# Kernel optimization log

Measured on AMD Instinct MI355X. Metric: run time of the kernel, lower is better.

The kernel has to match this reference:

```python
import jax, jax.numpy as jnp
import numpy as np

N, H, D, HDIM, HID = 768, 4, 3, 64, 64


def setup_inputs() -> dict:
    key = jax.random.key(0)
    ks = jax.random.split(key, 12)

    def w(k, shape, scale=None):
        s = (1.0 / np.sqrt(shape[0])) if scale is None else scale
        return (jax.random.normal(k, shape, jnp.float32) * s).astype(jnp.float32)

    d_in_e = H + 2 * (HDIM + H * H)  # 4 + 2*(64+16) = 164
    return {
        "x": jax.random.normal(ks[0], (N, H, D), jnp.float32),
        "h": jax.random.normal(ks[1], (N, HDIM), jnp.float32),
        "phi_e_w0": w(ks[2], (d_in_e, HID)), "phi_e_b0": jnp.zeros((HID,), jnp.float32),
        "phi_e_w1": w(ks[3], (HID, HID)), "phi_e_b1": jnp.zeros((HID,), jnp.float32),
        "phi_inf_w": w(ks[4], (HID, 1)), "phi_inf_b": jnp.zeros((1,), jnp.float32),
        "phi_x_w0": w(ks[5], (HID, HID)), "phi_x_b0": jnp.zeros((HID,), jnp.float32),
        "phi_x_w1": w(ks[6], (HID, HID)), "phi_x_b1": jnp.zeros((HID,), jnp.float32),
        "phi_x_w2": w(ks[7], (HID, H), scale=0.001), "phi_x_b2": jnp.zeros((H,), jnp.float32),
        "phi_h_w0": w(ks[8], (HID + HDIM, HID)), "phi_h_b0": jnp.zeros((HID,), jnp.float32),
        "phi_h_w1": w(ks[9], (HID, HID)), "phi_h_b1": jnp.zeros((HID,), jnp.float32),
        "phi_h_w2": w(ks[10], (HID, HDIM)), "phi_h_b2": jnp.zeros((HDIM,), jnp.float32),
    }


def _mlp2(z, w0, b0, w1, b1):
    # hk.nets.MLP([HID, HID], activation=silu, activate_final=True)
    return jax.nn.silu(jax.nn.silu(z @ w0 + b0) @ w1 + b1)


def reference(x, h,
              phi_e_w0, phi_e_b0, phi_e_w1, phi_e_b1,
              phi_inf_w, phi_inf_b,
              phi_x_w0, phi_x_b0, phi_x_w1, phi_x_b1, phi_x_w2, phi_x_b2,
              phi_h_w0, phi_h_b0, phi_h_w1, phi_h_b1, phi_h_w2, phi_h_b2):
    n, n_heads = x.shape[0], x.shape[1]
    avg_num_neighbours = n - 1
    off_n = 1.0 - jnp.eye(n, dtype=x.dtype)          # zero node-diagonal mask

    # per-node head-pair differences: [n, H, H, 3], entry [m,i,j] = x[m,j]-x[m,i]
    diff_heads = x[:, None, :, :] - x[:, :, None, :]
    sq_norms_heads = jnp.sum(diff_heads ** 2, axis=-1)            # [n, H, H]
    h_concat = jnp.concatenate([h, sq_norms_heads.reshape(n, n_heads * n_heads)], axis=-1)

    # all-pairs node features: [n, n, 2*(HDIM+H^2)], entry [i,j] = [h_concat[j], h_concat[i]]
    hc_dim = h_concat.shape[-1]
    h_combos = jnp.concatenate([
        jnp.broadcast_to(h_concat[None, :, :], (n, n, hc_dim)),
        jnp.broadcast_to(h_concat[:, None, :], (n, n, hc_dim)),
    ], axis=-1)

    # all-pairs node differences per head: [n, n, H, 3], entry [i,j] = x[j]-x[i]
    diff_nodes = x[None, :, :, :] - x[:, None, :, :]
    sq_norms_nodes = jnp.sum(diff_nodes ** 2, axis=-1)            # [n, n, H]

    e_in = jnp.concatenate([sq_norms_nodes, h_combos], axis=-1)   # [n, n, 164]
    m_ij = _mlp2(e_in, phi_e_w0, phi_e_b0, phi_e_w1, phi_e_b1)    # [n, n, HID]
    m_ij = m_ij * off_n[:, :, None]

    e = jax.nn.sigmoid(m_ij @ phi_inf_w + phi_inf_b)[..., 0] * off_n  # [n, n]
    m_i = jnp.einsum('ijd,ij->id', m_ij, e) / jnp.sqrt(jnp.asarray(avg_num_neighbours, x.dtype))

    # phi_x: MLP(silu, activate_final) -> Linear(H) (tanh=False)
    phi_x_out = (_mlp2(m_ij, phi_x_w0, phi_x_b0, phi_x_w1, phi_x_b1) @ phi_x_w2 + phi_x_b2)
    phi_x_out = phi_x_out * off_n[:, :, None]                     # [n, n, H]

    # normalize_by_x_norm=True, normalization_constant=1.0
    norm = jnp.sqrt(jnp.where(sq_norms_nodes == 0.0, 1.0, sq_norms_nodes)) + 1.0
    norm_diff = (diff_nodes / norm[..., None]) * off_n[:, :, None, None]
    equivariant_shift = jnp.einsum('ijhd,ijh->ihd', norm_diff, phi_x_out)
    equivariant_shift = equivariant_shift / avg_num_neighbours    # agg='mean'

    x_new = x + equivariant_shift

    phi_h_in = jnp.concatenate([m_i, h], axis=-1)
    h_new = _mlp2(phi_h_in, phi_h_w0, phi_h_b0, phi_h_w1, phi_h_b1) @ phi_h_w2 + phi_h_b2
    h_new = h + h_new                                             # residual_h=True
    return (x_new, h_new)
```

## Files before the change

### kernel.cpp

```cpp
#include <hip/hip_runtime.h>
#include <hip/hip_bf16.h>
#include <math.h>

#define WS_BJ    0
#define WS_BI    49152
#define WS_W0AT  98304
#define WS_BIAS  98560
#define WS_INFW  98784
#define WS_WG    98848
#define WS_PM    106016
#define WS_PS    253472

typedef unsigned short ushort_t;
typedef __attribute__((ext_vector_type(8))) __bf16 bf16x8;
typedef __attribute__((ext_vector_type(4))) float f32x4;

__device__ __forceinline__ float silu_f(float v) {
    return v * __builtin_amdgcn_rcpf(1.0f + __expf(-v));
}
__device__ __forceinline__ float sigm_f(float v) {
    return __builtin_amdgcn_rcpf(1.0f + __expf(-v));
}

__device__ __forceinline__ ushort_t bf16r(float f) {
    unsigned u = __float_as_uint(f);
    u += 0x7FFFu + ((u >> 16) & 1u);
    return (ushort_t)(u >> 16);
}
__device__ __forceinline__ float bf2f(ushort_t s) { return __uint_as_float(((unsigned)s) << 16); }

__device__ __forceinline__ unsigned pk2(float a, float b) {
    __hip_bfloat162 t = __float22bfloat162_rn(make_float2(a, b));
    return *reinterpret_cast<unsigned*>(&t);
}

__global__ __launch_bounds__(256) void prep_kernel(
    const float* __restrict__ x, const float* __restrict__ h,
    const float* __restrict__ ew0, const float* __restrict__ eb0,
    const float* __restrict__ ew1, const float* __restrict__ eb1,
    const float* __restrict__ infw, const float* __restrict__ infb,
    const float* __restrict__ xw0, const float* __restrict__ xb0,
    const float* __restrict__ xw1, const float* __restrict__ xb1,
    const float* __restrict__ xw2, const float* __restrict__ xb2,
    float* __restrict__ ws)
{
    const int blk = blockIdx.x, tid = threadIdx.x;
    const int wv = tid >> 6, t = tid & 63;
    if (blk < 192) {
        __shared__ float hcs[4][80];
        const int m = blk * 4 + wv;
        hcs[wv][t] = h[m * 64 + t];
        if (t < 16) {
            int i2 = t >> 2, j2 = t & 3;
            float d0 = x[m*12 + j2*3 + 0] - x[m*12 + i2*3 + 0];
            float d1 = x[m*12 + j2*3 + 1] - x[m*12 + i2*3 + 1];
            float d2 = x[m*12 + j2*3 + 2] - x[m*12 + i2*3 + 2];
            hcs[wv][64 + t] = d0*d0 + d1*d1 + d2*d2;
        }
        float bj = 0.0f, bi = eb0[t];
        #pragma unroll 4
        for (int k = 0; k < 80; ++k) {
            float hv = hcs[wv][k];
            bj += hv * ew0[(4 + k) * 64 + t];
            bi += hv * ew0[(84 + k) * 64 + t];
        }
        ws[WS_BJ + m * 64 + t] = bj;
        ws[WS_BI + m * 64 + t] = bi;
    } else if (blk == 192) {
        if (wv == 0) {
            #pragma unroll
            for (int hh = 0; hh < 4; ++hh) ws[WS_W0AT + t * 4 + hh] = ew0[hh * 64 + t];
            ws[WS_INFW + t] = infw[t];
            #pragma unroll
            for (int u = 0; u < 4; ++u) {
                int idx = u * 64 + t;
                if (idx < 224) {
                    float v;
                    if (idx < 64)        v = eb1[idx];
                    else if (idx < 128)  v = xb0[idx - 64];
                    else if (idx == 128) v = infb[0];
                    else if (idx < 144)  v = 0.0f;
                    else if (idx < 208)  v = xb1[idx - 144];
                    else if (idx < 212)  v = xb2[idx - 208];
                    else                 v = 0.0f;
                    ws[WS_BIAS + idx] = v;
                }
            }
        }
    } else {
        ushort_t* wg = (ushort_t*)(ws + WS_WG);
        #pragma unroll 1
        for (int u = 0; u < 8; ++u) {
            int e = (blk - 193) * 2048 + tid * 8 + u;
            int r = e >> 6, k = e & 63;
            float v;
            if (r < 64)        v = ew1[k * 64 + r];
            else if (r < 128)  v = xw0[k * 64 + (r - 64)];
            else if (r == 128) v = infw[k];
            else if (r < 144)  v = 0.0f;
            else if (r < 208)  v = xw1[k * 64 + (r - 144)];
            else if (r < 212)  v = xw2[k * 4 + (r - 208)];
            else               v = 0.0f;
            wg[e] = bf16r(v);
        }
    }
}

__device__ __forceinline__ void load_bfrags(const ushort_t* yb, int ml, int q, bf16x8 B[4][2]) {
    #pragma unroll
    for (int pt = 0; pt < 4; ++pt)
        #pragma unroll
        for (int kt = 0; kt < 2; ++kt)
            B[pt][kt] = *(const bf16x8*)(yb + (pt*16 + ml) * 72 + kt*32 + q*8);
}

template<int NMT>
__device__ __forceinline__ void gemmG(const ushort_t* __restrict__ wg, int ml, int q,
                                      const bf16x8 B[4][2], f32x4* acc) {
    #pragma unroll
    for (int mt = 0; mt < NMT; ++mt) {
        #pragma unroll
        for (int kt = 0; kt < 2; ++kt) {
            bf16x8 af = *(const bf16x8*)(wg + (mt*16 + ml) * 64 + kt*32 + q*8);
            #pragma unroll
            for (int pt = 0; pt < 4; ++pt)
                acc[mt*4 + pt] = __builtin_amdgcn_mfma_f32_16x16x32_bf16(af, B[pt][kt], acc[mt*4 + pt], 0, 0, 0);
        }
    }
}

__device__ __forceinline__ void ep_silu2(ushort_t* yb, int ml, int q,
                                         const f32x4* acc, const float* __restrict__ bias,
                                         int coff) {
    #pragma unroll
    for (int mt = 0; mt < 2; ++mt) {
        float4 bv = *(const float4*)(bias + coff + mt*16 + q*4);
        #pragma unroll
        for (int pt = 0; pt < 4; ++pt) {
            f32x4 a = acc[mt*4 + pt];
            uint2 w = make_uint2(pk2(silu_f(a[0] + bv.x), silu_f(a[1] + bv.y)),
                                 pk2(silu_f(a[2] + bv.z), silu_f(a[3] + bv.w)));
            *(uint2*)(yb + (pt*16 + ml) * 72 + coff + mt*16 + q*4) = w;
        }
    }
}

__device__ __forceinline__ void layer64(ushort_t* yb, const ushort_t* __restrict__ wg,
                                        const float* __restrict__ bias, int ml, int q) {
    bf16x8 B[4][2];
    load_bfrags(yb, ml, q, B);
    f32x4 acc[8];
    #pragma unroll
    for (int t = 0; t < 8; ++t) acc[t] = f32x4{0.f, 0.f, 0.f, 0.f};
    gemmG<2>(wg, ml, q, B, acc);
    ep_silu2(yb, ml, q, acc, bias, 0);
    #pragma unroll
    for (int t = 0; t < 8; ++t) acc[t] = f32x4{0.f, 0.f, 0.f, 0.f};
    gemmG<2>(wg + 32*64, ml, q, B, acc);
    ep_silu2(yb, ml, q, acc, bias, 32);
}

__global__ __launch_bounds__(256, 2) void egcl_chunk(
    const float* __restrict__ x, float* __restrict__ ws)
{
    __shared__ ushort_t ybuf[4][4608];
    __shared__ float sbuf[4][64];
    __shared__ float redm[4][64];
    __shared__ float reds[4][12];

    const int it = blockIdx.x, i = blockIdx.y, tid = threadIdx.x;
    const int wv = tid >> 6, lane = tid & 63;
    const int ml = lane & 15, q = lane >> 4;
    const int jg = it * 256 + wv * 64 + lane;

    const ushort_t* wg = (const ushort_t*)(ws + WS_WG);
    const float* bias  = ws + WS_BIAS;
    const float* infwf = ws + WS_INFW;
    ushort_t* yb = ybuf[wv];

    float xi[12];
    #pragma unroll
    for (int t = 0; t < 12; ++t) xi[t] = x[i * 12 + t];

    float sqn[4];
    {
        const float4* xp = (const float4*)(x + jg * 12);
        float4 a = xp[0], b = xp[1], c = xp[2];
        float d0, d1, d2;
        d0=a.x-xi[0]; d1=a.y-xi[1]; d2=a.z-xi[2];   sqn[0]=d0*d0+d1*d1+d2*d2;
        d0=a.w-xi[3]; d1=b.x-xi[4]; d2=b.y-xi[5];   sqn[1]=d0*d0+d1*d1+d2*d2;
        d0=b.z-xi[6]; d1=b.w-xi[7]; d2=c.x-xi[8];   sqn[2]=d0*d0+d1*d1+d2*d2;
        d0=c.y-xi[9]; d1=c.z-xi[10];d2=c.w-xi[11];  sqn[3]=d0*d0+d1*d1+d2*d2;
    }

    {
        const float* Bi   = ws + WS_BI + i * 64;
        const float* w0at = ws + WS_W0AT;
        const float* Bj   = ws + WS_BJ + jg * 64;
        #pragma unroll
        for (int b = 0; b < 8; ++b) {
            float4 A = *(const float4*)(Bj + b*8);
            float4 Bv = *(const float4*)(Bj + b*8 + 4);
            float z[8] = {A.x, A.y, A.z, A.w, Bv.x, Bv.y, Bv.z, Bv.w};
            #pragma unroll
            for (int u = 0; u < 8; ++u) {
                int l = b*8 + u;
                float v = Bi[l] + z[u]
                        + sqn[0]*w0at[l*4+0] + sqn[1]*w0at[l*4+1]
                        + sqn[2]*w0at[l*4+2] + sqn[3]*w0at[l*4+3];
                z[u] = silu_f(v);
            }
            uint4 pkv = make_uint4(pk2(z[0],z[1]), pk2(z[2],z[3]),
                                   pk2(z[4],z[5]), pk2(z[6],z[7]));
            *(uint4*)(yb + lane * 72 + b*8) = pkv;
        }
    }

    layer64(yb, wg + 0, bias + 0, ml, q);

    {
        float sv = bias[128];
        #pragma unroll
        for (int c = 0; c < 8; ++c) {
            uint2 w0 = *(const uint2*)(yb + lane * 72 + c*8);
            uint2 w1 = *(const uint2*)(yb + lane * 72 + c*8 + 4);
            sv += __uint_as_float(w0.x << 16)          * infwf[c*8 + 0];
            sv += __uint_as_float(w0.x & 0xFFFF0000u)  * infwf[c*8 + 1];
            sv += __uint_as_float(w0.y << 16)          * infwf[c*8 + 2];
            sv += __uint_as_float(w0.y & 0xFFFF0000u)  * infwf[c*8 + 3];
            sv += __uint_as_float(w1.x << 16)          * infwf[c*8 + 4];
            sv += __uint_as_float(w1.x & 0xFFFF0000u)  * infwf[c*8 + 5];
            sv += __uint_as_float(w1.y << 16)          * infwf[c*8 + 6];
            sv += __uint_as_float(w1.y & 0xFFFF0000u)  * infwf[c*8 + 7];
        }
        sbuf[wv][lane] = (jg == i) ? 0.0f : sigm_f(sv);
    }

    float macc = 0.0f;
    #pragma unroll 8
    for (int j2 = 0; j2 < 64; ++j2) {
        float ev = sbuf[wv][j2];
        macc += ev * bf2f(yb[j2 * 72 + lane]);
    }

    layer64(yb, wg + 64*64, bias + 64, ml, q);
    layer64(yb, wg + 144*64, bias + 144, ml, q);

    float* yf = (float*)yb;
    {
        bf16x8 B[4][2];
        load_bfrags(yb, ml, q, B);
        f32x4 acc2[4];
        #pragma unroll
        for (int t = 0; t < 4; ++t) acc2[t] = f32x4{0.f, 0.f, 0.f, 0.f};
        gemmG<1>(wg + 208*64, ml, q, B, acc2);
        if (q == 0) {
            float4 bx2 = *(const float4*)(bias + 208);
            #pragma unroll
            for (int pt = 0; pt < 4; ++pt) {
                float4 pv = make_float4(acc2[pt][0] + bx2.x, acc2[pt][1] + bx2.y,
                                        acc2[pt][2] + bx2.z, acc2[pt][3] + bx2.w);
                *(float4*)(yf + (pt*16 + ml) * 4) = pv;
            }
        }
    }

    {
        float4 pv = *(const float4*)(yf + lane * 4);
        float pvh[4] = {pv.x, pv.y, pv.z, pv.w};
        float mask = (jg == i) ? 0.0f : 1.0f;
        const float4* xp = (const float4*)(x + jg * 12);
        float4 a = xp[0], b = xp[1], c = xp[2];
        float dxs[12];
        dxs[0]=a.x-xi[0]; dxs[1]=a.y-xi[1]; dxs[2]=a.z-xi[2];  dxs[3]=a.w-xi[3];
        dxs[4]=b.x-xi[4]; dxs[5]=b.y-xi[5]; dxs[6]=b.z-xi[6];  dxs[7]=b.w-xi[7];
        dxs[8]=c.x-xi[8]; dxs[9]=c.y-xi[9]; dxs[10]=c.z-xi[10];dxs[11]=c.w-xi[11];
        float s12[12];
        #pragma unroll
        for (int hh = 0; hh < 4; ++hh) {
            float nsq = (sqn[hh] == 0.0f) ? 1.0f : sqn[hh];
            float inv = mask * pvh[hh] * __builtin_amdgcn_rcpf(sqrtf(nsq) + 1.0f);
            #pragma unroll
            for (int d = 0; d < 3; ++d)
                s12[hh*3 + d] = dxs[hh*3 + d] * inv;
        }
        #pragma unroll
        for (int t = 0; t < 12; ++t) {
            float v = s12[t];
            v += __shfl_xor(v, 1, 64);
            v += __shfl_xor(v, 2, 64);
            v += __shfl_xor(v, 4, 64);
            v += __shfl_xor(v, 8, 64);
            v += __shfl_xor(v, 16, 64);
            v += __shfl_xor(v, 32, 64);
            if (lane == 0) reds[wv][t] = v;
        }
    }

    redm[wv][lane] = macc;
    __syncthreads();

    if (wv == 0) {
        ws[WS_PM + (i*3 + it)*64 + lane] =
            redm[0][lane] + redm[1][lane] + redm[2][lane] + redm[3][lane];
        if (lane < 12)
            ws[WS_PS + (i*3 + it)*12 + lane] =
                reds[0][lane] + reds[1][lane] + reds[2][lane] + reds[3][lane];
    }
}

__global__ __launch_bounds__(256) void finish_kernel(
    const float* __restrict__ x, const float* __restrict__ h,
    const float* __restrict__ hw0, const float* __restrict__ hb0,
    const float* __restrict__ hw1, const float* __restrict__ hb1,
    const float* __restrict__ hw2, const float* __restrict__ hb2,
    const float* __restrict__ ws, float* __restrict__ out)
{
    __shared__ float inbuf[4][128];
    __shared__ float zbuf[4][64];
    const int tid = threadIdx.x;
    const int wv = tid >> 6, lane = tid & 63;
    const int i = blockIdx.x * 4 + wv;

    const float* pm = ws + WS_PM + i*3*64;
    float mi = (pm[lane] + pm[64 + lane] + pm[128 + lane]) * (1.0f / sqrtf(767.0f));
    inbuf[wv][lane] = mi;
    inbuf[wv][64 + lane] = h[i*64 + lane];

    if (lane < 12) {
        const float* ps = ws + WS_PS + i*3*12;
        float sh = ps[lane] + ps[12 + lane] + ps[24 + lane];
        out[i*12 + lane] = x[i*12 + lane] + sh * (1.0f / 767.0f);
    }

    float a = hb0[lane];
    #pragma unroll 8
    for (int k = 0; k < 128; ++k) a += inbuf[wv][k] * hw0[k*64 + lane];
    zbuf[wv][lane] = silu_f(a);

    a = hb1[lane];
    #pragma unroll 8
    for (int k = 0; k < 64; ++k) a += zbuf[wv][k] * hw1[k*64 + lane];
    zbuf[wv][lane] = silu_f(a);

    a = hb2[lane];
    #pragma unroll 8
    for (int k = 0; k < 64; ++k) a += zbuf[wv][k] * hw2[k*64 + lane];
    out[9216 + i*64 + lane] = h[i*64 + lane] + a;
}

extern "C" void kernel_launch(void* const* d_in, const int* in_sizes, int n_in,
                              void* d_out, int out_size, void* d_ws, size_t ws_size,
                              hipStream_t stream) {
    const float* x    = (const float*)d_in[0];
    const float* h    = (const float*)d_in[1];
    const float* ew0  = (const float*)d_in[2];
    const float* eb0  = (const float*)d_in[3];
    const float* ew1  = (const float*)d_in[4];
    const float* eb1  = (const float*)d_in[5];
    const float* infw = (const float*)d_in[6];
    const float* infb = (const float*)d_in[7];
    const float* xw0  = (const float*)d_in[8];
    const float* xb0  = (const float*)d_in[9];
    const float* xw1  = (const float*)d_in[10];
    const float* xb1  = (const float*)d_in[11];
    const float* xw2  = (const float*)d_in[12];
    const float* xb2  = (const float*)d_in[13];
    const float* hw0  = (const float*)d_in[14];
    const float* hb0  = (const float*)d_in[15];
    const float* hw1  = (const float*)d_in[16];
    const float* hb1  = (const float*)d_in[17];
    const float* hw2  = (const float*)d_in[18];
    const float* hb2  = (const float*)d_in[19];

    float* ws  = (float*)d_ws;
    float* out = (float*)d_out;

    prep_kernel<<<200, 256, 0, stream>>>(x, h, ew0, eb0, ew1, eb1, infw, infb,
                                         xw0, xb0, xw1, xb1, xw2, xb2, ws);
    egcl_chunk<<<dim3(3, 768), 256, 0, stream>>>(x, ws);
    finish_kernel<<<192, 256, 0, stream>>>(x, h, hw0, hb0, hw1, hb1, hw2, hb2, ws, out);
}
```

Baseline: 171.8 us.

## Swizzle LDS activation tiles, fold bias into MFMA accumulators, use 192-thread blocks

```diff
diff --git a/kernel.cpp b/kernel.cpp
--- a/kernel.cpp
+++ b/kernel.cpp
@@ -9,7 +9,7 @@
 #define WS_INFW  98784
 #define WS_WG    98848
 #define WS_PM    106016
-#define WS_PS    253472
+#define WS_PS    302624
 
 typedef unsigned short ushort_t;
 typedef __attribute__((ext_vector_type(8))) __bf16 bf16x8;
@@ -32,6 +32,13 @@
 __device__ __forceinline__ unsigned pk2(float a, float b) {
     __hip_bfloat162 t = __float22bfloat162_rn(make_float2(a, b));
     return *reinterpret_cast<unsigned*>(&t);
+}
+
+__device__ __forceinline__ int ybo(int row, int slot) {
+    return row * 64 + (((slot) ^ (row & 7)) << 3);
+}
+__device__ __forceinline__ int yfo(int row) {
+    return row * 32 + ((row & 7) << 2);
 }
 
 __global__ __launch_bounds__(256) void prep_kernel(
@@ -111,7 +118,7 @@
     for (int pt = 0; pt < 4; ++pt)
         #pragma unroll
         for (int kt = 0; kt < 2; ++kt)
-            B[pt][kt] = *(const bf16x8*)(yb + (pt*16 + ml) * 72 + kt*32 + q*8);
+            B[pt][kt] = *(const bf16x8*)(yb + ybo(pt*16 + ml, kt*4 + q));
 }
 
 template<int NMT>
@@ -130,17 +137,17 @@
 }
 
 __device__ __forceinline__ void ep_silu2(ushort_t* yb, int ml, int q,
-                                         const f32x4* acc, const float* __restrict__ bias,
-                                         int coff) {
+                                         const f32x4* acc, int coff) {
     #pragma unroll
     for (int mt = 0; mt < 2; ++mt) {
-        float4 bv = *(const float4*)(bias + coff + mt*16 + q*4);
         #pragma unroll
         for (int pt = 0; pt < 4; ++pt) {
             f32x4 a = acc[mt*4 + pt];
-            uint2 w = make_uint2(pk2(silu_f(a[0] + bv.x), silu_f(a[1] + bv.y)),
-                                 pk2(silu_f(a[2] + bv.z), silu_f(a[3] + bv.w)));
-            *(uint2*)(yb + (pt*16 + ml) * 72 + coff + mt*16 + q*4) = w;
+            uint2 w = make_uint2(pk2(silu_f(a[0]), silu_f(a[1])),
+                                 pk2(silu_f(a[2]), silu_f(a[3])));
+            int row  = pt*16 + ml;
+            int slot = (coff >> 3) + mt*2 + (q >> 1);
+            *(uint2*)(yb + ybo(row, slot) + (q & 1) * 4) = w;
         }
     }
 }
@@ -151,27 +158,35 @@
     load_bfrags(yb, ml, q, B);
     f32x4 acc[8];
     #pragma unroll
-    for (int t = 0; t < 8; ++t) acc[t] = f32x4{0.f, 0.f, 0.f, 0.f};
+    for (int mt = 0; mt < 2; ++mt) {
+        float4 bv = *(const float4*)(bias + mt*16 + q*4);
+        #pragma unroll
+        for (int pt = 0; pt < 4; ++pt) acc[mt*4 + pt] = f32x4{bv.x, bv.y, bv.z, bv.w};
+    }
     gemmG<2>(wg, ml, q, B, acc);
-    ep_silu2(yb, ml, q, acc, bias, 0);
-    #pragma unroll
-    for (int t = 0; t < 8; ++t) acc[t] = f32x4{0.f, 0.f, 0.f, 0.f};
+    ep_silu2(yb, ml, q, acc, 0);
+    #pragma unroll
+    for (int mt = 0; mt < 2; ++mt) {
+        float4 bv = *(const float4*)(bias + 32 + mt*16 + q*4);
+        #pragma unroll
+        for (int pt = 0; pt < 4; ++pt) acc[mt*4 + pt] = f32x4{bv.x, bv.y, bv.z, bv.w};
+    }
     gemmG<2>(wg + 32*64, ml, q, B, acc);
-    ep_silu2(yb, ml, q, acc, bias, 32);
-}
-
-__global__ __launch_bounds__(256, 2) void egcl_chunk(
+    ep_silu2(yb, ml, q, acc, 32);
+}
+
+__global__ __launch_bounds__(192, 4) void egcl_chunk(
     const float* __restrict__ x, float* __restrict__ ws)
 {
-    __shared__ ushort_t ybuf[4][4608];
-    __shared__ float sbuf[4][64];
-    __shared__ float redm[4][64];
-    __shared__ float reds[4][12];
+    __shared__ __align__(16) ushort_t ybuf[3][4096];
+    __shared__ float sbuf[3][64];
+    __shared__ float redm[3][64];
+    __shared__ float reds[3][12];
 
     const int it = blockIdx.x, i = blockIdx.y, tid = threadIdx.x;
     const int wv = tid >> 6, lane = tid & 63;
     const int ml = lane & 15, q = lane >> 4;
-    const int jg = it * 256 + wv * 64 + lane;
+    const int jg = it * 192 + wv * 64 + lane;
 
     const ushort_t* wg = (const ushort_t*)(ws + WS_WG);
     const float* bias  = ws + WS_BIAS;
@@ -212,7 +227,7 @@
             }
             uint4 pkv = make_uint4(pk2(z[0],z[1]), pk2(z[2],z[3]),
                                    pk2(z[4],z[5]), pk2(z[6],z[7]));
-            *(uint4*)(yb + lane * 72 + b*8) = pkv;
+            *(uint4*)(yb + ybo(lane, b)) = pkv;
         }
     }
 
@@ -222,8 +237,9 @@
         float sv = bias[128];
         #pragma unroll
         for (int c = 0; c < 8; ++c) {
-            uint2 w0 = *(const uint2*)(yb + lane * 72 + c*8);
-            uint2 w1 = *(const uint2*)(yb + lane * 72 + c*8 + 4);
+            int base = ybo(lane, c);
+            uint2 w0 = *(const uint2*)(yb + base);
+            uint2 w1 = *(const uint2*)(yb + base + 4);
             sv += __uint_as_float(w0.x << 16)          * infwf[c*8 + 0];
             sv += __uint_as_float(w0.x & 0xFFFF0000u)  * infwf[c*8 + 1];
             sv += __uint_as_float(w0.y << 16)          * infwf[c*8 + 2];
@@ -237,10 +253,13 @@
     }
 
     float macc = 0.0f;
-    #pragma unroll 8
-    for (int j2 = 0; j2 < 64; ++j2) {
-        float ev = sbuf[wv][j2];
-        macc += ev * bf2f(yb[j2 * 72 + lane]);
+    {
+        const int g = lane >> 3, l7 = lane & 7;
+        #pragma unroll 8
+        for (int j2 = 0; j2 < 64; ++j2) {
+            float ev = sbuf[wv][j2];
+            macc += ev * bf2f(yb[j2*64 + (((g ^ (j2 & 7)) << 3) + l7)]);
+        }
     }
 
     layer64(yb, wg + 64*64, bias + 64, ml, q);
@@ -251,22 +270,22 @@
         bf16x8 B[4][2];
         load_bfrags(yb, ml, q, B);
         f32x4 acc2[4];
-        #pragma unroll
-        for (int t = 0; t < 4; ++t) acc2[t] = f32x4{0.f, 0.f, 0.f, 0.f};
+        float4 bx2 = *(const float4*)(bias + 208);
+        #pragma unroll
+        for (int t = 0; t < 4; ++t) acc2[t] = f32x4{bx2.x, bx2.y, bx2.z, bx2.w};
         gemmG<1>(wg + 208*64, ml, q, B, acc2);
         if (q == 0) {
-            float4 bx2 = *(const float4*)(bias + 208);
             #pragma unroll
             for (int pt = 0; pt < 4; ++pt) {
-                float4 pv = make_float4(acc2[pt][0] + bx2.x, acc2[pt][1] + bx2.y,
-                                        acc2[pt][2] + bx2.z, acc2[pt][3] + bx2.w);
-                *(float4*)(yf + (pt*16 + ml) * 4) = pv;
+                int row = pt*16 + ml;
+                *(float4*)(yf + yfo(row)) =
+                    make_float4(acc2[pt][0], acc2[pt][1], acc2[pt][2], acc2[pt][3]);
             }
         }
     }
 
     {
-        float4 pv = *(const float4*)(yf + lane * 4);
+        float4 pv = *(const float4*)(yf + yfo(lane));
         float pvh[4] = {pv.x, pv.y, pv.z, pv.w};
         float mask = (jg == i) ? 0.0f : 1.0f;
         const float4* xp = (const float4*)(x + jg * 12);
@@ -301,11 +320,11 @@
     __syncthreads();
 
     if (wv == 0) {
-        ws[WS_PM + (i*3 + it)*64 + lane] =
-            redm[0][lane] + redm[1][lane] + redm[2][lane] + redm[3][lane];
+        ws[WS_PM + (i*4 + it)*64 + lane] =
+            redm[0][lane] + redm[1][lane] + redm[2][lane];
         if (lane < 12)
-            ws[WS_PS + (i*3 + it)*12 + lane] =
-                reds[0][lane] + reds[1][lane] + reds[2][lane] + reds[3][lane];
+            ws[WS_PS + (i*4 + it)*12 + lane] =
+                reds[0][lane] + reds[1][lane] + reds[2][lane];
     }
 }
 
@@ -322,14 +341,15 @@
     const int wv = tid >> 6, lane = tid & 63;
     const int i = blockIdx.x * 4 + wv;
 
-    const float* pm = ws + WS_PM + i*3*64;
-    float mi = (pm[lane] + pm[64 + lane] + pm[128 + lane]) * (1.0f / sqrtf(767.0f));
+    const float* pm = ws + WS_PM + i*4*64;
+    float mi = (pm[lane] + pm[64 + lane] + pm[128 + lane] + pm[192 + lane])
+               * (1.0f / sqrtf(767.0f));
     inbuf[wv][lane] = mi;
     inbuf[wv][64 + lane] = h[i*64 + lane];
 
     if (lane < 12) {
-        const float* ps = ws + WS_PS + i*3*12;
-        float sh = ps[lane] + ps[12 + lane] + ps[24 + lane];
+        const float* ps = ws + WS_PS + i*4*12;
+        float sh = ps[lane] + ps[12 + lane] + ps[24 + lane] + ps[36 + lane];
         out[i*12 + lane] = x[i*12 + lane] + sh * (1.0f / 767.0f);
     }
 
@@ -378,6 +398,6 @@
 
     prep_kernel<<<200, 256, 0, stream>>>(x, h, ew0, eb0, ew1, eb1, infw, infb,
                                          xw0, xb0, xw1, xb1, xw2, xb2, ws);
-    egcl_chunk<<<dim3(3, 768), 256, 0, stream>>>(x, ws);
+    egcl_chunk<<<dim3(4, 768), 192, 0, stream>>>(x, ws);
     finish_kernel<<<192, 256, 0, stream>>>(x, h, hw0, hb0, hw1, hb1, hw2, hb2, ws, out);
 }
```

After: 173.7 us. Within noise of the previous version (+1.1%).

## Compute edge gate via MFMA and reuse B fragments for phi_x layer

Applied to the files above, without the earlier changes.

```diff
diff --git a/kernel.cpp b/kernel.cpp
--- a/kernel.cpp
+++ b/kernel.cpp
@@ -175,22 +175,23 @@
 
     const ushort_t* wg = (const ushort_t*)(ws + WS_WG);
     const float* bias  = ws + WS_BIAS;
-    const float* infwf = ws + WS_INFW;
     ushort_t* yb = ybuf[wv];
 
-    float xi[12];
-    #pragma unroll
-    for (int t = 0; t < 12; ++t) xi[t] = x[i * 12 + t];
-
+    float dxs[12];
     float sqn[4];
     {
+        float xi[12];
+        #pragma unroll
+        for (int t = 0; t < 12; ++t) xi[t] = x[i * 12 + t];
         const float4* xp = (const float4*)(x + jg * 12);
         float4 a = xp[0], b = xp[1], c = xp[2];
-        float d0, d1, d2;
-        d0=a.x-xi[0]; d1=a.y-xi[1]; d2=a.z-xi[2];   sqn[0]=d0*d0+d1*d1+d2*d2;
-        d0=a.w-xi[3]; d1=b.x-xi[4]; d2=b.y-xi[5];   sqn[1]=d0*d0+d1*d1+d2*d2;
-        d0=b.z-xi[6]; d1=b.w-xi[7]; d2=c.x-xi[8];   sqn[2]=d0*d0+d1*d1+d2*d2;
-        d0=c.y-xi[9]; d1=c.z-xi[10];d2=c.w-xi[11];  sqn[3]=d0*d0+d1*d1+d2*d2;
+        dxs[0]=a.x-xi[0]; dxs[1]=a.y-xi[1]; dxs[2]=a.z-xi[2];  dxs[3]=a.w-xi[3];
+        dxs[4]=b.x-xi[4]; dxs[5]=b.y-xi[5]; dxs[6]=b.z-xi[6];  dxs[7]=b.w-xi[7];
+        dxs[8]=c.x-xi[8]; dxs[9]=c.y-xi[9]; dxs[10]=c.z-xi[10];dxs[11]=c.w-xi[11];
+        #pragma unroll
+        for (int hh = 0; hh < 4; ++hh)
+            sqn[hh] = dxs[hh*3+0]*dxs[hh*3+0] + dxs[hh*3+1]*dxs[hh*3+1]
+                    + dxs[hh*3+2]*dxs[hh*3+2];
     }
 
     {
@@ -218,22 +219,23 @@
 
     layer64(yb, wg + 0, bias + 0, ml, q);
 
-    {
-        float sv = bias[128];
-        #pragma unroll
-        for (int c = 0; c < 8; ++c) {
-            uint2 w0 = *(const uint2*)(yb + lane * 72 + c*8);
-            uint2 w1 = *(const uint2*)(yb + lane * 72 + c*8 + 4);
-            sv += __uint_as_float(w0.x << 16)          * infwf[c*8 + 0];
-            sv += __uint_as_float(w0.x & 0xFFFF0000u)  * infwf[c*8 + 1];
-            sv += __uint_as_float(w0.y << 16)          * infwf[c*8 + 2];
-            sv += __uint_as_float(w0.y & 0xFFFF0000u)  * infwf[c*8 + 3];
-            sv += __uint_as_float(w1.x << 16)          * infwf[c*8 + 4];
-            sv += __uint_as_float(w1.x & 0xFFFF0000u)  * infwf[c*8 + 5];
-            sv += __uint_as_float(w1.y << 16)          * infwf[c*8 + 6];
-            sv += __uint_as_float(w1.y & 0xFFFF0000u)  * infwf[c*8 + 7];
-        }
-        sbuf[wv][lane] = (jg == i) ? 0.0f : sigm_f(sv);
+    bf16x8 Bm[4][2];
+    load_bfrags(yb, ml, q, Bm);
+
+    {
+        f32x4 acc2[4];
+        #pragma unroll
+        for (int t = 0; t < 4; ++t) acc2[t] = f32x4{0.f, 0.f, 0.f, 0.f};
+        gemmG<1>(wg + 128*64, ml, q, Bm, acc2);
+        if (q == 0) {
+            #pragma unroll
+            for (int pt = 0; pt < 4; ++pt) {
+                int p  = pt*16 + ml;
+                int jj = it*256 + wv*64 + p;
+                float sv = acc2[pt][0] + bias[128];
+                sbuf[wv][p] = (jj == i) ? 0.0f : sigm_f(sv);
+            }
+        }
     }
 
     float macc = 0.0f;
@@ -243,7 +245,18 @@
         macc += ev * bf2f(yb[j2 * 72 + lane]);
     }
 
-    layer64(yb, wg + 64*64, bias + 64, ml, q);
+    {
+        f32x4 acc[8];
+        #pragma unroll
+        for (int t = 0; t < 8; ++t) acc[t] = f32x4{0.f, 0.f, 0.f, 0.f};
+        gemmG<2>(wg + 64*64, ml, q, Bm, acc);
+        ep_silu2(yb, ml, q, acc, bias + 64, 0);
+        #pragma unroll
+        for (int t = 0; t < 8; ++t) acc[t] = f32x4{0.f, 0.f, 0.f, 0.f};
+        gemmG<2>(wg + 64*64 + 32*64, ml, q, Bm, acc);
+        ep_silu2(yb, ml, q, acc, bias + 64, 32);
+    }
+
     layer64(yb, wg + 144*64, bias + 144, ml, q);
 
     float* yf = (float*)yb;
@@ -269,12 +282,6 @@
         float4 pv = *(const float4*)(yf + lane * 4);
         float pvh[4] = {pv.x, pv.y, pv.z, pv.w};
         float mask = (jg == i) ? 0.0f : 1.0f;
-        const float4* xp = (const float4*)(x + jg * 12);
-        float4 a = xp[0], b = xp[1], c = xp[2];
-        float dxs[12];
-        dxs[0]=a.x-xi[0]; dxs[1]=a.y-xi[1]; dxs[2]=a.z-xi[2];  dxs[3]=a.w-xi[3];
-        dxs[4]=b.x-xi[4]; dxs[5]=b.y-xi[5]; dxs[6]=b.z-xi[6];  dxs[7]=b.w-xi[7];
-        dxs[8]=c.x-xi[8]; dxs[9]=c.y-xi[9]; dxs[10]=c.z-xi[10];dxs[11]=c.w-xi[11];
         float s12[12];
         #pragma unroll
         for (int hh = 0; hh < 4; ++hh) {
```

Result: no change. 170.4 us, median of 2 (-0.8%).
